# Kernel optimization log

Hardware: AMD Instinct MI355X
Metric: run time of the kernel (lower is better)

## Reference

```python
import jax, jax.numpy as jnp
import numpy as np

EMBED_DIM = 1024
NUM_HEADS = 16
HEAD_DIM = EMBED_DIM // NUM_HEADS
ROPE_BASE = 10000.0
SQK_INIT_VALUE = 1.0
SQK_INIT_SCALING = 1.0 / (EMBED_DIM ** 0.5)


def setup_inputs() -> dict:
    key = jax.random.key(0)
    ks = jax.random.split(key, 6)
    B, N = 1, 2048
    x = jax.random.normal(ks[0], (B, N, EMBED_DIM), dtype=jnp.float32)
    # torch nn.Linear weights are [out_features, in_features]; y = x @ W.T
    s = EMBED_DIM ** -0.5
    Wq = jax.random.normal(ks[1], (EMBED_DIM, EMBED_DIM), dtype=jnp.float32) * s
    Wk = jax.random.normal(ks[2], (EMBED_DIM, EMBED_DIM), dtype=jnp.float32) * s
    Wv = jax.random.normal(ks[3], (EMBED_DIM, EMBED_DIM), dtype=jnp.float32) * s
    Wo = jax.random.normal(ks[4], (EMBED_DIM, EMBED_DIM), dtype=jnp.float32) * s
    sqk = SQK_INIT_SCALING * jnp.ones((EMBED_DIM,), dtype=jnp.float32) \
        + 0.01 * jax.random.normal(ks[5], (EMBED_DIM,), dtype=jnp.float32)
    return {"x": x, "Wq": Wq, "Wk": Wk, "Wv": Wv, "Wo": Wo, "sqk": sqk}


def _rope(t, offset=0):
    # t: [b, h, n, d]; rotary position embedding (Lrpe type 1), half-split layout
    d = t.shape[-1]
    n = t.shape[-2]
    inv_freq = 1.0 / (ROPE_BASE ** (jnp.arange(0, d, 2, dtype=jnp.float32) / d))  # [d/2]
    pos = jnp.arange(n, dtype=jnp.float32) + offset                               # [n]
    freqs = pos[:, None] * inv_freq[None, :]                                      # [n, d/2]
    cos = jnp.cos(freqs)
    sin = jnp.sin(freqs)
    t1, t2 = jnp.split(t, 2, axis=-1)
    return jnp.concatenate([t1 * cos - t2 * sin, t1 * sin + t2 * cos], axis=-1)


def _justnorm(t):
    return t / jnp.linalg.norm(t, axis=-1, keepdims=True)


def reference(x, Wq, Wk, Wv, Wo, sqk):
    B, N, E = x.shape
    H, D = NUM_HEADS, HEAD_DIM
    q = jnp.einsum('bne,fe->bnf', x, Wq).reshape(B, N, H, D).transpose(0, 2, 1, 3)
    k = jnp.einsum('bne,fe->bnf', x, Wk).reshape(B, N, H, D).transpose(0, 2, 1, 3)
    v = jnp.einsum('bne,fe->bnf', x, Wv).reshape(B, N, H, D).transpose(0, 2, 1, 3)
    q = _rope(q)
    k = _rope(k)
    # sqk * (init_value / init_scaling), reshaped to (h, 1, d)
    sqk_s = (sqk * (SQK_INIT_VALUE / SQK_INIT_SCALING)).reshape(H, 1, D)
    q = sqk_s * _justnorm(q)
    k = sqk_s * _justnorm(k)
    # SDPA with scale = sqrt(head_dim) (as in the source), causal
    scale = D ** 0.5
    scores = jnp.einsum('bhnd,bhmd->bhnm', q, k) * scale
    causal = jnp.tril(jnp.ones((N, N), dtype=bool))
    scores = jnp.where(causal, scores, -jnp.inf)
    attn = jax.nn.softmax(scores, axis=-1)
    out = jnp.einsum('bhnm,bhmd->bhnd', attn, v)           # [b,h,n,d]
    out = out.transpose(0, 2, 1, 3).reshape(B, N, E)       # [b,n,e]
    out = jnp.einsum('bne,fe->bnf', out, Wo)
    return out
```

## Files before the change

### kernel.cpp

```cpp
#include <hip/hip_runtime.h>
#include <hip/hip_bf16.h>

typedef float f32x4 __attribute__((ext_vector_type(4)));
typedef __bf16 bf16x8 __attribute__((ext_vector_type(8)));
typedef __bf16 bf16x4 __attribute__((ext_vector_type(4)));

__device__ __forceinline__ void gload_lds16(const __bf16* g, __bf16* l) {
  __builtin_amdgcn_global_load_lds(
      (const __attribute__((address_space(1))) void*)g,
      (__attribute__((address_space(3))) void*)l, 16, 0, 0);
}

__global__ __launch_bounds__(256) void convert_all(
    const float* __restrict__ x, const float* __restrict__ wq,
    const float* __restrict__ wk, const float* __restrict__ wv,
    const float* __restrict__ wo, __bf16* __restrict__ dst)
{
  int t = blockIdx.x * 256 + threadIdx.x;
  const float* src; size_t soff;
  if (t < 262144) { src = x; soff = (size_t)t * 8; }
  else {
    int r = (t - 262144) >> 17;
    src = (r == 0) ? wq : (r == 1) ? wk : (r == 2) ? wv : wo;
    soff = (size_t)((t - 262144) & 131071) * 8;
  }
  float4 f0 = *(const float4*)(src + soff);
  float4 f1 = *(const float4*)(src + soff + 4);
  bf16x8 o;
  o[0]=(__bf16)f0.x; o[1]=(__bf16)f0.y; o[2]=(__bf16)f0.z; o[3]=(__bf16)f0.w;
  o[4]=(__bf16)f1.x; o[5]=(__bf16)f1.y; o[6]=(__bf16)f1.z; o[7]=(__bf16)f1.w;
  *(bf16x8*)(dst + (size_t)t * 8) = o;
}

template <int BM, int BN, int BK, typename OutT, bool ROPE>
__global__ __launch_bounds__(256) void gemm_bt(
    const __bf16* __restrict__ A,
    const __bf16* __restrict__ B0, const __bf16* __restrict__ B1, const __bf16* __restrict__ B2,
    OutT* __restrict__ C0, OutT* __restrict__ C1, OutT* __restrict__ C2,
    int M, int N, int K, const float* __restrict__ sqkp)
{
  const __bf16* B = (blockIdx.z == 0) ? B0 : (blockIdx.z == 1) ? B1 : B2;
  OutT* C = (blockIdx.z == 0) ? C0 : (blockIdx.z == 1) ? C1 : C2;

  constexpr int MT = BM / 32, NT = BN / 32, KK = BK / 32;
  constexpr int CPR = BK / 8;
  constexpr int RPI = 64 / CPR;
  __shared__ __align__(16) __bf16 As[BM * BK];
  __shared__ __align__(16) __bf16 Bs[BN * BK];

  const int tid = threadIdx.x, w = tid >> 6, l = tid & 63;
  const int wr = w >> 1, wc = w & 1;
  const int g = l >> 4, c16 = l & 15;
  const int bm = blockIdx.y, bn = blockIdx.x;
  const int lr = l / CPR, lc = l % CPR;

  f32x4 acc[MT][NT] = {};
  const int nk = K / BK;

  for (int kt = 0; kt < nk; ++kt) {
    __syncthreads();
#pragma unroll
    for (int i = w; i < BM / RPI; i += 4) {
      int row = i * RPI + lr;
      int sch = lc ^ (row & 7);
      gload_lds16(A + (size_t)(bm * BM + row) * K + kt * BK + sch * 8, As + i * RPI * BK);
    }
#pragma unroll
    for (int i = w; i < BN / RPI; i += 4) {
      int row = i * RPI + lr;
      int sch = lc ^ (row & 7);
      gload_lds16(B + (size_t)(bn * BN + row) * K + kt * BK + sch * 8, Bs + i * RPI * BK);
    }
    __syncthreads();

#pragma unroll
    for (int kk = 0; kk < KK; ++kk) {
      bf16x8 af[MT], bf[NT];
#pragma unroll
      for (int mt = 0; mt < MT; ++mt) {
        int row = wr * (BM / 2) + mt * 16 + c16;
        af[mt] = *(const bf16x8*)(As + row * BK + (((kk * 4 + g) ^ (row & 7)) * 8));
      }
#pragma unroll
      for (int nt = 0; nt < NT; ++nt) {
        int row = wc * (BN / 2) + nt * 16 + c16;
        bf[nt] = *(const bf16x8*)(Bs + row * BK + (((kk * 4 + g) ^ (row & 7)) * 8));
      }
#pragma unroll
      for (int mt = 0; mt < MT; ++mt)
#pragma unroll
        for (int nt = 0; nt < NT; ++nt)
          acc[mt][nt] = __builtin_amdgcn_mfma_f32_16x16x32_bf16(af[mt], bf[nt], acc[mt][nt], 0, 0, 0);
    }
  }

  bool done = false;
  if constexpr (ROPE) {
    static_assert(!ROPE || NT == 4, "ROPE epilogue assumes BN=128");
    if (blockIdx.z < 2) {
      const bool isQ = (blockIdx.z == 0);
      const int hcol = bn * BN + wc * (BN / 2);
      float sq[4];
#pragma unroll
      for (int nt = 0; nt < 4; ++nt) sq[nt] = sqkp[hcol + nt * 16 + c16] * 32.0f;
      const float QSC = 8.0f * 1.4426950408889634f;
      const float L = 0.415241011860919f;
      const float inv0 = exp2f(-(float)c16 * L);
      const float inv1 = exp2f(-(float)(c16 + 16) * L);
#pragma unroll
      for (int mt = 0; mt < MT; ++mt) {
#pragma unroll
        for (int r = 0; r < 4; ++r) {
          int row = bm * BM + wr * (BM / 2) + mt * 16 + g * 4 + r;
          float s0, c0, s1, c1;
          sincosf((float)row * inv0, &s0, &c0);
          sincosf((float)row * inv1, &s1, &c1);
          float v0 = acc[mt][0][r], v1 = acc[mt][1][r];
          float v2 = acc[mt][2][r], v3 = acc[mt][3][r];
          float n0 = v0 * c0 - v2 * s0;
          float n2 = v0 * s0 + v2 * c0;
          float n1 = v1 * c1 - v3 * s1;
          float n3 = v1 * s1 + v3 * c1;
          float ss = n0 * n0 + n1 * n1 + n2 * n2 + n3 * n3;
#pragma unroll
          for (int m2 = 1; m2 < 16; m2 <<= 1) ss += __shfl_xor(ss, m2, 16);
          float rinv = rsqrtf(ss);
          if (isQ) rinv *= QSC;
          C[(size_t)row * N + hcol +  0 + c16] = (OutT)(n0 * sq[0] * rinv);
          C[(size_t)row * N + hcol + 16 + c16] = (OutT)(n1 * sq[1] * rinv);
          C[(size_t)row * N + hcol + 32 + c16] = (OutT)(n2 * sq[2] * rinv);
          C[(size_t)row * N + hcol + 48 + c16] = (OutT)(n3 * sq[3] * rinv);
        }
      }
      done = true;
    }
  }
  if (!done) {
#pragma unroll
    for (int mt = 0; mt < MT; ++mt)
#pragma unroll
      for (int nt = 0; nt < NT; ++nt)
#pragma unroll
        for (int r = 0; r < 4; ++r) {
          int row = bm * BM + wr * (BM / 2) + mt * 16 + g * 4 + r;
          int col = bn * BN + wc * (BN / 2) + nt * 16 + c16;
          C[(size_t)row * N + col] = (OutT)acc[mt][nt][r];
        }
  }
}

__global__ __launch_bounds__(256) void vtrans(const __bf16* __restrict__ v, __bf16* __restrict__ vt)
{
  __shared__ __align__(16) __bf16 t[64 * 72];
  int h = blockIdx.y;
  int n0 = blockIdx.x * 64;
  int tid = threadIdx.x;
#pragma unroll
  for (int j = 0; j < 2; ++j) {
    int idx = tid + j * 256;
    int r = idx >> 3, c = (idx & 7) * 8;
    bf16x8 val = *(const bf16x8*)(v + (size_t)(n0 + r) * 1024 + h * 64 + c);
    *(bf16x8*)&t[r * 72 + c] = val;
  }
  __syncthreads();
#pragma unroll
  for (int j = 0; j < 2; ++j) {
    int idx = tid + j * 256;
    int d = idx >> 3, nn = (idx & 7) * 8;
    bf16x8 o;
#pragma unroll
    for (int jj = 0; jj < 8; ++jj) o[jj] = t[(nn + jj) * 72 + d];
    *(bf16x8*)(vt + (size_t)(h * 64 + d) * 2048 + n0 + nn) = o;
  }
}

#define STAGE(BUF, KT)                                                         \
  {                                                                            \
    _Pragma("unroll")                                                          \
    for (int p = 0; p < 2; ++p) {                                              \
      int row = srow + p * 32;                                                 \
      int sch = sc ^ (row & 7);                                                \
      gload_lds16(Kg + (size_t)((KT) * 64 + row) * 1024 + h * 64 + sch * 8,    \
                  &Ks[BUF][w * 512 + p * 2048]);                               \
      gload_lds16(Vg + ((size_t)h * 64 + row) * 2048 + (KT) * 64 + sch * 8,    \
                  &Vs[BUF][w * 512 + p * 2048]);                               \
    }                                                                          \
  }

__global__ __launch_bounds__(256, 4) void attn_kernel(
    const __bf16* __restrict__ Qg, const __bf16* __restrict__ Kg,
    const __bf16* __restrict__ Vg, __bf16* __restrict__ Og,
    float* __restrict__ oS, float* __restrict__ lS)
{
  __shared__ __align__(16) __bf16 Ks[2][4096];
  __shared__ __align__(16) __bf16 Vs[2][4096];
  __shared__ __align__(16) __bf16 Ps[4][1024];

  const int b = blockIdx.x;
  int h, qt, kts, kte, sidx;
  if (b < 512) {
    int p = b >> 5;
    qt = 16 + p;
    sidx = (b >> 4) & 1;
    h = b & 15;
    int mid = (qt + 1) >> 1;
    kts = sidx ? mid : 0;
    kte = sidx ? qt : (mid - 1);
  } else {
    qt = 15 - ((b - 512) >> 4);
    h = b & 15;
    kts = 0; kte = qt; sidx = -1;
  }
  const int q0 = qt * 64;

  const int tid = threadIdx.x, w = tid >> 6, l = tid & 63;
  const int g = l >> 4, c16 = l & 15;
  const int srow = tid >> 3;
  const int sc   = tid & 7;
  const int swz  = (c16 & 7) << 4;

  __bf16* Ps_w = &Ps[w][0];
  const int qig = q0 + w * 16 + c16;

  const __bf16* qbase = Qg + (size_t)qig * 1024 + h * 64 + g * 8;
  const bf16x8 qf0 = *(const bf16x8*)(qbase);
  const bf16x8 qf1 = *(const bf16x8*)(qbase + 32);

  bf16x8 onesf;
#pragma unroll
  for (int j = 0; j < 8; ++j) onesf[j] = (__bf16)1.0f;

  f32x4 o[4] = {};
  f32x4 ol = {};

  STAGE(0, kts)

  for (int kt = kts; kt <= kte; ++kt) {
    const int cur = (kt - kts) & 1;
    __syncthreads();
    if (kt < kte) STAGE(cur ^ 1, kt + 1)

    const __bf16* Kb = Ks[cur];
    const __bf16* Vb = Vs[cur];

    __builtin_amdgcn_s_setprio(1);
    f32x4 s[4] = {};
#pragma unroll
    for (int kjb = 0; kjb < 4; ++kjb) {
      int r = kjb * 16 + c16;
      bf16x8 k0 = *(const bf16x8*)((char*)Kb + r * 128 + ((g ^ (r & 7)) * 16));
      bf16x8 k1 = *(const bf16x8*)((char*)Kb + r * 128 + (((4 + g) ^ (r & 7)) * 16));
      s[kjb] = __builtin_amdgcn_mfma_f32_16x16x32_bf16(k0, qf0, s[kjb], 0, 0, 0);
      s[kjb] = __builtin_amdgcn_mfma_f32_16x16x32_bf16(k1, qf1, s[kjb], 0, 0, 0);
    }
    __builtin_amdgcn_s_setprio(0);

    const bool diag = (kt == qt);
#pragma unroll
    for (int kjb = 0; kjb < 4; ++kjb) {
      bf16x4 pk;
#pragma unroll
      for (int r = 0; r < 4; ++r) {
        float sv = s[kjb][r];
        int kvg = kt * 64 + kjb * 16 + g * 4 + r;
        if (diag && kvg > qig) sv = -1e30f;
        pk[r] = (__bf16)exp2f(sv);
      }
      int pbyte = (c16 * 128 + kjb * 32 + g * 8) ^ swz;
      *(bf16x4*)((char*)Ps_w + pbyte) = pk;
    }

    __builtin_amdgcn_s_setprio(1);
#pragma unroll
    for (int ks = 0; ks < 2; ++ks) {
      int abyte = (c16 * 128 + ks * 64 + g * 16) ^ swz;
      bf16x8 pa = *(const bf16x8*)((char*)Ps_w + abyte);
#pragma unroll
      for (int nt = 0; nt < 4; ++nt) {
        int r = nt * 16 + c16;
        bf16x8 vb = *(const bf16x8*)((char*)Vb + r * 128 + (((ks * 4 + g) ^ (r & 7)) * 16));
        o[nt] = __builtin_amdgcn_mfma_f32_16x16x32_bf16(pa, vb, o[nt], 0, 0, 0);
      }
      ol = __builtin_amdgcn_mfma_f32_16x16x32_bf16(pa, onesf, ol, 0, 0, 0);
    }
    __builtin_amdgcn_s_setprio(0);
  }

  if (sidx < 0) {
#pragma unroll
    for (int r = 0; r < 4; ++r) {
      float rinv = 1.0f / ol[r];
      int qi = q0 + w * 16 + g * 4 + r;
#pragma unroll
      for (int nt = 0; nt < 4; ++nt)
        Og[(size_t)qi * 1024 + h * 64 + nt * 16 + c16] = (__bf16)(o[nt][r] * rinv);
    }
  } else {
    float* oBase = oS + (size_t)sidx * 1024 * 1024;
#pragma unroll
    for (int r = 0; r < 4; ++r) {
      int row = q0 + w * 16 + g * 4 + r - 1024;
#pragma unroll
      for (int nt = 0; nt < 4; ++nt)
        oBase[(size_t)row * 1024 + h * 64 + nt * 16 + c16] = o[nt][r];
      if (c16 == 0)
        lS[(size_t)sidx * 1024 * 16 + (size_t)row * 16 + h] = ol[r];
    }
  }
}

__global__ __launch_bounds__(256) void merge_halves(
    const float* __restrict__ oS, const float* __restrict__ lS,
    __bf16* __restrict__ Og)
{
  int row = blockIdx.x;
  int col = threadIdx.x * 4;
  int h = col >> 6;
  float lsum = lS[(size_t)row * 16 + h] + lS[(size_t)(1024 + row) * 16 + h];
  float rinv = 1.0f / lsum;
  f32x4 a = *(const f32x4*)(oS + (size_t)row * 1024 + col);
  f32x4 bb = *(const f32x4*)(oS + (size_t)(1024 * 1024) + (size_t)row * 1024 + col);
  f32x4 sum = a + bb;
  bf16x4 ob;
  ob[0] = (__bf16)(sum[0] * rinv); ob[1] = (__bf16)(sum[1] * rinv);
  ob[2] = (__bf16)(sum[2] * rinv); ob[3] = (__bf16)(sum[3] * rinv);
  *(bf16x4*)(Og + (size_t)(1024 + row) * 1024 + col) = ob;
}

extern "C" void kernel_launch(void* const* d_in, const int* in_sizes, int n_in,
                              void* d_out, int out_size, void* d_ws, size_t ws_size,
                              hipStream_t stream) {
  const float* x   = (const float*)d_in[0];
  const float* Wq  = (const float*)d_in[1];
  const float* Wk  = (const float*)d_in[2];
  const float* Wv  = (const float*)d_in[3];
  const float* Wo  = (const float*)d_in[4];
  const float* sqk = (const float*)d_in[5];
  float* out = (float*)d_out;

  __bf16* xb  = (__bf16*)d_ws;
  __bf16* wqb = xb  + (size_t)2048 * 1024;
  __bf16* wkb = wqb + (size_t)1024 * 1024;
  __bf16* wvb = wkb + (size_t)1024 * 1024;
  __bf16* wob = wvb + (size_t)1024 * 1024;
  __bf16* qn  = wob + (size_t)1024 * 1024;
  __bf16* kn  = qn  + (size_t)2048 * 1024;
  __bf16* v   = kn  + (size_t)2048 * 1024;
  __bf16* vtb = v   + (size_t)2048 * 1024;
  __bf16* og  = vtb + (size_t)2048 * 1024;
  float*  oS  = (float*)(og + (size_t)2048 * 1024);
  float*  lS  = oS + (size_t)2 * 1024 * 1024;

  convert_all<<<3072, 256, 0, stream>>>(x, Wq, Wk, Wv, Wo, xb);
  gemm_bt<64, 128, 64, __bf16, true><<<dim3(8, 32, 3), 256, 0, stream>>>(
      xb, wqb, wkb, wvb, qn, kn, v, 2048, 1024, 1024, sqk);
  vtrans<<<dim3(32, 16), 256, 0, stream>>>(v, vtb);
  attn_kernel<<<768, 256, 0, stream>>>(qn, kn, vtb, og, oS, lS);
  merge_halves<<<1024, 256, 0, stream>>>(oS, lS, og);
  gemm_bt<64, 64, 64, float, false><<<dim3(16, 32, 1), 256, 0, stream>>>(
      og, wob, wob, wob, out, out, out, 2048, 1024, 1024, nullptr);
}
```

Measured before the change: 77.98 us.

## Fuse split-KV merge into output projection GEMM and tighten attention barriers

Removes the separate merge_halves kernel. The output-projection GEMM now reads the two fp32 partial attention outputs and their row sums directly for rows in the second half, normalises them, converts to bf16 and writes the A tile into LDS. This saves one launch and a bf16 round trip through global memory, but it replaces the async global-to-LDS load for those tiles with synchronous fp32 loads that read twice the bytes. Separately, the attention loop swaps __syncthreads for explicit barriers with partial vmcnt waits so the next stage's prefetch can stay in flight, and it drops the setprio hints.

```diff
diff --git a/kernel.cpp b/kernel.cpp
--- a/kernel.cpp
+++ b/kernel.cpp
@@ -32,12 +32,13 @@
   *(bf16x8*)(dst + (size_t)t * 8) = o;
 }
 
-template <int BM, int BN, int BK, typename OutT, bool ROPE>
+template <int BM, int BN, int BK, typename OutT, bool ROPE, bool MERGE>
 __global__ __launch_bounds__(256) void gemm_bt(
     const __bf16* __restrict__ A,
     const __bf16* __restrict__ B0, const __bf16* __restrict__ B1, const __bf16* __restrict__ B2,
     OutT* __restrict__ C0, OutT* __restrict__ C1, OutT* __restrict__ C2,
-    int M, int N, int K, const float* __restrict__ sqkp)
+    int M, int N, int K, const float* __restrict__ sqkp,
+    const float* __restrict__ oS, const float* __restrict__ lS)
 {
   const __bf16* B = (blockIdx.z == 0) ? B0 : (blockIdx.z == 1) ? B1 : B2;
   OutT* C = (blockIdx.z == 0) ? C0 : (blockIdx.z == 1) ? C1 : C2;
@@ -56,14 +57,36 @@
 
   f32x4 acc[MT][NT] = {};
   const int nk = K / BK;
+  const bool amerge = MERGE && (bm >= 16);
 
   for (int kt = 0; kt < nk; ++kt) {
     __syncthreads();
-#pragma unroll
-    for (int i = w; i < BM / RPI; i += 4) {
-      int row = i * RPI + lr;
-      int sch = lc ^ (row & 7);
-      gload_lds16(A + (size_t)(bm * BM + row) * K + kt * BK + sch * 8, As + i * RPI * BK);
+    if (amerge) {
+#pragma unroll
+      for (int ii = 0; ii < 2; ++ii) {
+        int row = (w + ii * 4) * 8 + (l >> 3);
+        int sr = bm * 64 + row - 1024;
+        int ch = (l & 7) ^ (row & 7);
+        const float* pa0 = oS + (size_t)sr * 1024 + kt * 64 + ch * 8;
+        f32x4 a0 = *(const f32x4*)(pa0);
+        f32x4 a1 = *(const f32x4*)(pa0 + 4);
+        f32x4 b0 = *(const f32x4*)(pa0 + 1024 * 1024);
+        f32x4 b1 = *(const f32x4*)(pa0 + 1024 * 1024 + 4);
+        float rinv = 1.0f / (lS[(size_t)sr * 16 + kt] + lS[(size_t)16384 + sr * 16 + kt]);
+        a0 = (a0 + b0) * rinv;
+        a1 = (a1 + b1) * rinv;
+        bf16x8 pk;
+        pk[0]=(__bf16)a0[0]; pk[1]=(__bf16)a0[1]; pk[2]=(__bf16)a0[2]; pk[3]=(__bf16)a0[3];
+        pk[4]=(__bf16)a1[0]; pk[5]=(__bf16)a1[1]; pk[6]=(__bf16)a1[2]; pk[7]=(__bf16)a1[3];
+        *(bf16x8*)(As + row * BK + (l & 7) * 8) = pk;
+      }
+    } else {
+#pragma unroll
+      for (int i = w; i < BM / RPI; i += 4) {
+        int row = i * RPI + lr;
+        int sch = lc ^ (row & 7);
+        gload_lds16(A + (size_t)(bm * BM + row) * K + kt * BK + sch * 8, As + i * RPI * BK);
+      }
     }
 #pragma unroll
     for (int i = w; i < BN / RPI; i += 4) {
@@ -237,13 +260,20 @@
 
   for (int kt = kts; kt <= kte; ++kt) {
     const int cur = (kt - kts) & 1;
-    __syncthreads();
-    if (kt < kte) STAGE(cur ^ 1, kt + 1)
+    __builtin_amdgcn_s_barrier();
+    __builtin_amdgcn_sched_barrier(0);
+    if (kt < kte) {
+      STAGE(cur ^ 1, kt + 1)
+      asm volatile("s_waitcnt vmcnt(4)" ::: "memory");
+    } else {
+      asm volatile("s_waitcnt vmcnt(0)" ::: "memory");
+    }
+    __builtin_amdgcn_s_barrier();
+    __builtin_amdgcn_sched_barrier(0);
 
     const __bf16* Kb = Ks[cur];
     const __bf16* Vb = Vs[cur];
 
-    __builtin_amdgcn_s_setprio(1);
     f32x4 s[4] = {};
 #pragma unroll
     for (int kjb = 0; kjb < 4; ++kjb) {
@@ -253,7 +283,6 @@
       s[kjb] = __builtin_amdgcn_mfma_f32_16x16x32_bf16(k0, qf0, s[kjb], 0, 0, 0);
       s[kjb] = __builtin_amdgcn_mfma_f32_16x16x32_bf16(k1, qf1, s[kjb], 0, 0, 0);
     }
-    __builtin_amdgcn_s_setprio(0);
 
     const bool diag = (kt == qt);
 #pragma unroll
@@ -270,7 +299,6 @@
       *(bf16x4*)((char*)Ps_w + pbyte) = pk;
     }
 
-    __builtin_amdgcn_s_setprio(1);
 #pragma unroll
     for (int ks = 0; ks < 2; ++ks) {
       int abyte = (c16 * 128 + ks * 64 + g * 16) ^ swz;
@@ -283,7 +311,6 @@
       }
       ol = __builtin_amdgcn_mfma_f32_16x16x32_bf16(pa, onesf, ol, 0, 0, 0);
     }
-    __builtin_amdgcn_s_setprio(0);
   }
 
   if (sidx < 0) {
@@ -307,24 +334,6 @@
         lS[(size_t)sidx * 1024 * 16 + (size_t)row * 16 + h] = ol[r];
     }
   }
-}
-
-__global__ __launch_bounds__(256) void merge_halves(
-    const float* __restrict__ oS, const float* __restrict__ lS,
-    __bf16* __restrict__ Og)
-{
-  int row = blockIdx.x;
-  int col = threadIdx.x * 4;
-  int h = col >> 6;
-  float lsum = lS[(size_t)row * 16 + h] + lS[(size_t)(1024 + row) * 16 + h];
-  float rinv = 1.0f / lsum;
-  f32x4 a = *(const f32x4*)(oS + (size_t)row * 1024 + col);
-  f32x4 bb = *(const f32x4*)(oS + (size_t)(1024 * 1024) + (size_t)row * 1024 + col);
-  f32x4 sum = a + bb;
-  bf16x4 ob;
-  ob[0] = (__bf16)(sum[0] * rinv); ob[1] = (__bf16)(sum[1] * rinv);
-  ob[2] = (__bf16)(sum[2] * rinv); ob[3] = (__bf16)(sum[3] * rinv);
-  *(bf16x4*)(Og + (size_t)(1024 + row) * 1024 + col) = ob;
 }
 
 extern "C" void kernel_launch(void* const* d_in, const int* in_sizes, int n_in,
@@ -352,11 +361,10 @@
   float*  lS  = oS + (size_t)2 * 1024 * 1024;
 
   convert_all<<<3072, 256, 0, stream>>>(x, Wq, Wk, Wv, Wo, xb);
-  gemm_bt<64, 128, 64, __bf16, true><<<dim3(8, 32, 3), 256, 0, stream>>>(
-      xb, wqb, wkb, wvb, qn, kn, v, 2048, 1024, 1024, sqk);
+  gemm_bt<64, 128, 64, __bf16, true, false><<<dim3(8, 32, 3), 256, 0, stream>>>(
+      xb, wqb, wkb, wvb, qn, kn, v, 2048, 1024, 1024, sqk, nullptr, nullptr);
   vtrans<<<dim3(32, 16), 256, 0, stream>>>(v, vtb);
   attn_kernel<<<768, 256, 0, stream>>>(qn, kn, vtb, og, oS, lS);
-  merge_halves<<<1024, 256, 0, stream>>>(oS, lS, og);
-  gemm_bt<64, 64, 64, float, false><<<dim3(16, 32, 1), 256, 0, stream>>>(
-      og, wob, wob, wob, out, out, out, 2048, 1024, 1024, nullptr);
-}
+  gemm_bt<64, 64, 64, float, false, true><<<dim3(16, 32, 1), 256, 0, stream>>>(
+      og, wob, wob, wob, out, out, out, 2048, 1024, 1024, nullptr, oS, lS);
+}
```

Result: slower. 85.92 us (+10.2%).
